# Optimization experiments

Hardware: AMD Instinct MI355X
Metric: run time of the kernel (lower is better)

Reference implementation:

```python
import jax, jax.numpy as jnp
import numpy as np

B, T_MAX, D_MODEL, H, DH = 16, 4096, 1024, 16, 64


def _rope(x, positions):
    """Standard half-split RoPE. x: (B, T, H, Dh), positions: (T,) int32."""
    half = x.shape[-1] // 2
    inv_freq = 1.0 / (10000.0 ** (jnp.arange(half, dtype=jnp.float32) / half))
    ang = positions.astype(jnp.float32)[:, None] * inv_freq  # (T, half)
    cos = jnp.cos(ang)[None, :, None, :]  # (1, T, 1, half)
    sin = jnp.sin(ang)[None, :, None, :]
    x1, x2 = x[..., :half], x[..., half:]
    return jnp.concatenate([x1 * cos - x2 * sin, x1 * sin + x2 * cos], axis=-1)


def setup_inputs() -> dict:
    key = jax.random.key(0)
    ks = jax.random.split(key, 8)
    s_in = 1.0 / np.sqrt(D_MODEL)
    s_out = 1.0 / np.sqrt(H * DH)
    return {
        "x": jax.random.normal(ks[0], (B, 1, D_MODEL), jnp.float32),
        "cached_key": jax.random.normal(ks[1], (B, T_MAX, H, DH), jnp.float32),
        "cached_value": jax.random.normal(ks[2], (B, T_MAX, H, DH), jnp.float32),
        "Wq": jax.random.normal(ks[3], (D_MODEL, H, DH), jnp.float32) * s_in,
        "bq": jnp.zeros((H, DH), jnp.float32),
        "Wk": jax.random.normal(ks[4], (D_MODEL, H, DH), jnp.float32) * s_in,
        "bk": jnp.zeros((H, DH), jnp.float32),
        "Wv": jax.random.normal(ks[5], (D_MODEL, H, DH), jnp.float32) * s_in,
        "bv": jnp.zeros((H, DH), jnp.float32),
        "Wo": jax.random.normal(ks[6], (H, DH, D_MODEL), jnp.float32) * s_out,
        "bo": jnp.zeros((D_MODEL,), jnp.float32),
        "cache_index": 2047,
    }


def reference(x, cached_key, cached_value, Wq, bq, Wk, bk, Wv, bv, Wo, bo, cache_index):
    # QKV projections on the single decode token: (B, 1, H, Dh)
    q = jnp.einsum('bte,ehd->bthd', x, Wq) + bq
    k = jnp.einsum('bte,ehd->bthd', x, Wk) + bk
    v = jnp.einsum('bte,ehd->bthd', x, Wv) + bv

    # Scatter new K/V into the fixed cache at cache_index
    ck = cached_key.at[:, cache_index].set(k[:, 0])
    cv = cached_value.at[:, cache_index].set(v[:, 0])

    # RoPE: Q at position cache_index, K over the entire cache 0..T_max-1
    q_rot = _rope(q, jnp.array([cache_index], dtype=jnp.int32))
    k_rot = _rope(ck, jnp.arange(T_MAX, dtype=jnp.int32))

    # Masked single-query dot-product attention over valid slots
    scale = 1.0 / np.sqrt(DH).astype(np.float32)
    scores = jnp.einsum('bqhd,bkhd->bhqk', q_rot, k_rot) * scale  # (B, H, 1, T)
    slot_mask = jnp.arange(T_MAX) <= cache_index  # (T,)
    scores = jnp.where(slot_mask[None, None, None, :], scores, jnp.float32(-1e30))
    attn = jax.nn.softmax(scores, axis=-1)
    o = jnp.einsum('bhqk,bkhd->bqhd', attn, cv)  # (B, 1, H, Dh)

    # Output projection
    return jnp.einsum('bqhd,hde->bqe', o, Wo) + bo  # (B, 1, d_model)
```

## Files before the change

kernel.cpp:

```cpp
#include <hip/hip_runtime.h>
#include <math.h>

typedef float f4 __attribute__((ext_vector_type(4)));

#define B_    16
#define TMAX  4096
#define DM    1024
#define H_    16
#define DH    64
#define SPLIT 8
#define SCALE 0.125f
#define ROPE_L 0.28782313662425572f

#define WS_Q     0
#define WS_PO    16384
#define WS_PM    147456
#define WS_PL    149504
#define WS_OF    151552
#define WS_BIG   167936

__device__ __forceinline__ f4 ldnt(const f4* p) { return __builtin_nontemporal_load(p); }

__device__ __forceinline__ float wred_max(float v) {
#pragma unroll
    for (int o = 32; o > 0; o >>= 1) v = fmaxf(v, __shfl_xor(v, o, 64));
    return v;
}
__device__ __forceinline__ float wred_sum(float v) {
#pragma unroll
    for (int o = 32; o > 0; o >>= 1) v += __shfl_xor(v, o, 64);
    return v;
}

__global__ __launch_bounds__(256) void k_qkv(const float* __restrict__ x,
                      const float* __restrict__ Wq, const float* __restrict__ Wk,
                      const float* __restrict__ Wv, float* __restrict__ ws) {
    const int ec = blockIdx.x, h = blockIdx.y, mat = blockIdx.z;
    const float* W = (mat == 0) ? Wq : ((mat == 1) ? Wk : Wv);
    const int tid = threadIdx.x;
    const int d = tid & 63, es = tid >> 6;
    __shared__ float xs[B_][128];
    __shared__ float red[4][B_][64];
    for (int i = tid; i < B_ * 128; i += 256) {
        int b = i >> 7, e = i & 127;
        xs[b][e] = x[b * DM + ec * 128 + e];
    }
    __syncthreads();
    float acc[B_];
#pragma unroll
    for (int b = 0; b < B_; b++) acc[b] = 0.f;
    for (int i = 0; i < 32; i++) {
        int el = es * 32 + i;
        int e = ec * 128 + el;
        float w = W[((size_t)e * H_ + h) * DH + d];
#pragma unroll
        for (int b = 0; b < B_; b++) acc[b] += xs[b][el] * w;
    }
#pragma unroll
    for (int b = 0; b < B_; b++) red[es][b][d] = acc[b];
    __syncthreads();
    const int b4 = tid >> 6;
#pragma unroll
    for (int bb = 0; bb < 4; bb++) {
        int b = b4 * 4 + bb;
        float v = red[0][b][d] + red[1][b][d] + red[2][b][d] + red[3][b][d];
        ws[WS_BIG + (((size_t)(mat * 8 + ec) * B_ + b) * H_ + h) * DH + d] = v;
    }
}

__global__ void k_qkvred(float* __restrict__ cached_key, float* __restrict__ cached_value,
                         const float* __restrict__ bq, const float* __restrict__ bk,
                         const float* __restrict__ bv, const int* __restrict__ cidx,
                         float* __restrict__ ws) {
    const int bh = blockIdx.x, d = threadIdx.x;
    const int b = bh >> 4, h = bh & 15;
    const int P = *cidx;
    float q = bq[h * 64 + d], k = bk[h * 64 + d], v = bv[h * 64 + d];
    const float* big = ws + WS_BIG;
    const size_t matstride = (size_t)8 * B_ * H_ * DH;
#pragma unroll
    for (int ec = 0; ec < 8; ec++) {
        size_t base = (((size_t)ec * B_ + b) * H_ + h) * DH + d;
        q += big[base];
        k += big[matstride + base];
        v += big[2 * matstride + base];
    }
    ws[WS_Q + bh * 64 + d] = q;
    size_t off = (((size_t)b * TMAX + P) * H_ + h) * DH + d;
    cached_key[off] = k;
    cached_value[off] = v;
}

__global__ __launch_bounds__(256) void k_attn(const float* __restrict__ K,
                                              const float* __restrict__ V,
                                              const int* __restrict__ cidx,
                                              float* __restrict__ ws) {
    const int s = blockIdx.x, h = blockIdx.y, b = blockIdx.z;
    const int tid = threadIdx.x;
    const int P = *cidx;
    const int n = P + 1;
    const int chunk = (n + SPLIT - 1) / SPLIT;
    const int t0 = s * chunk;
    int t1 = t0 + chunk; if (t1 > n) t1 = n;
    const int len = (t1 > t0) ? (t1 - t0) : 0;
    const int bh = b * H_ + h;

    __shared__ float qr[64];
    __shared__ float sc[512];
    __shared__ float rb_m[4], rb_s[4];
    __shared__ float ov[16][64];

    if (tid < 64) {
        int d = tid;
        const float* qv = ws + WS_Q + bh * 64;
        int j = (d < 32) ? d : (d - 32);
        float invf = __expf(-(float)j * ROPE_L);
        float sn, c;
        sincosf((float)P * invf, &sn, &c);
        qr[d] = (d < 32) ? (qv[d] * c - qv[d + 32] * sn)
                         : (qv[d - 32] * sn + qv[d] * c);
    }
    __syncthreads();

    const int pos_sub = tid >> 3, q = tid & 7;
    float qa0 = qr[4 * q + 0], qa1 = qr[4 * q + 1], qa2 = qr[4 * q + 2], qa3 = qr[4 * q + 3];
    float qb0 = qr[4 * q + 32], qb1 = qr[4 * q + 33], qb2 = qr[4 * q + 34], qb3 = qr[4 * q + 35];
    float if0 = __expf(-(float)(4 * q + 0) * ROPE_L);
    float if1 = __expf(-(float)(4 * q + 1) * ROPE_L);
    float if2 = __expf(-(float)(4 * q + 2) * ROPE_L);
    float if3 = __expf(-(float)(4 * q + 3) * ROPE_L);

    float tmax = -3.0e38f;
    for (int base = 0; base < len; base += 32) {
        int idx = base + pos_sub;
        bool act = idx < len;
        int t = t0 + idx;
        f4 k1 = {0.f, 0.f, 0.f, 0.f}, k2 = {0.f, 0.f, 0.f, 0.f};
        if (act) {
            const f4* kp = (const f4*)(K + (((size_t)b * TMAX + t) * H_ + h) * DH);
            k1 = ldnt(kp + q);
            k2 = ldnt(kp + q + 8);
        }
        float tf = (float)t;
        float s0, c0, s1, c1, s2, c2, s3, c3;
        sincosf(tf * if0, &s0, &c0);
        sincosf(tf * if1, &s1, &c1);
        sincosf(tf * if2, &s2, &c2);
        sincosf(tf * if3, &s3, &c3);
        float p = k1.x * (qa0 * c0 + qb0 * s0) + k2.x * (qb0 * c0 - qa0 * s0)
                + k1.y * (qa1 * c1 + qb1 * s1) + k2.y * (qb1 * c1 - qa1 * s1)
                + k1.z * (qa2 * c2 + qb2 * s2) + k2.z * (qb2 * c2 - qa2 * s2)
                + k1.w * (qa3 * c3 + qb3 * s3) + k2.w * (qb3 * c3 - qa3 * s3);
#pragma unroll
        for (int o = 1; o < 8; o <<= 1) p += __shfl_xor(p, o, 64);
        if (act) {
            float sv = p * SCALE;
            if (q == 0) sc[idx] = sv;
            tmax = fmaxf(tmax, sv);
        }
    }
    float wm = wred_max(tmax);
    if ((tid & 63) == 0) rb_m[tid >> 6] = wm;
    __syncthreads();
    float m = fmaxf(fmaxf(rb_m[0], rb_m[1]), fmaxf(rb_m[2], rb_m[3]));

    float tsum = 0.f;
    for (int idx = tid; idx < len; idx += 256) {
        float pp = __expf(sc[idx] - m);
        sc[idx] = pp;
        tsum += pp;
    }
    float wsum = wred_sum(tsum);
    if ((tid & 63) == 0) rb_s[tid >> 6] = wsum;
    __syncthreads();
    float l = rb_s[0] + rb_s[1] + rb_s[2] + rb_s[3];

    const int d4 = tid & 15, grp = tid >> 4;
    f4 acc4 = {0.f, 0.f, 0.f, 0.f};
#pragma unroll 4
    for (int idx = grp; idx < len; idx += 16) {
        int t = t0 + idx;
        const f4* vp = (const f4*)(V + (((size_t)b * TMAX + t) * H_ + h) * DH) + d4;
        f4 vv = ldnt(vp);
        acc4 += sc[idx] * vv;
    }
    *(f4*)&ov[grp][d4 * 4] = acc4;
    __syncthreads();
    if (tid < 64) {
        float o = 0.f;
#pragma unroll
        for (int g = 0; g < 16; g++) o += ov[g][tid];
        ws[WS_PO + ((size_t)bh * SPLIT + s) * 64 + tid] = o;
        if (tid == 0) {
            ws[WS_PM + bh * SPLIT + s] = (len > 0) ? m : -1.0e30f;
            ws[WS_PL + bh * SPLIT + s] = l;
        }
    }
}

__global__ void k_combine(float* __restrict__ ws) {
    int bh = blockIdx.x;
    int d = threadIdx.x;
    const float* pm = ws + WS_PM + bh * SPLIT;
    const float* pl = ws + WS_PL + bh * SPLIT;
    const float* po = ws + WS_PO + (size_t)bh * SPLIT * 64;
    float m = -3.0e38f;
#pragma unroll
    for (int s = 0; s < SPLIT; s++) m = fmaxf(m, pm[s]);
    float l = 0.f, o = 0.f;
#pragma unroll
    for (int s = 0; s < SPLIT; s++) {
        float w = __expf(pm[s] - m);
        l += pl[s] * w;
        o += po[s * 64 + d] * w;
    }
    ws[WS_OF + bh * 64 + d] = o / l;
}

__global__ __launch_bounds__(256) void k_oproj(const float* __restrict__ Wo,
                        float* __restrict__ ws) {
    const int ec = blockIdx.x, hc = blockIdx.y;
    const int tid = threadIdx.x;
    const int el = tid & 63, grp = tid >> 6;
    const int e = ec * 64 + el;
    __shared__ float ofs[B_][64];
    __shared__ float red[4][B_][64];
    for (int i = tid; i < B_ * 64; i += 256) {
        int b = i >> 6, j = i & 63;
        ofs[b][j] = ws[WS_OF + b * (H_ * DH) + hc * 64 + j];
    }
    __syncthreads();
    float acc[B_];
#pragma unroll
    for (int b = 0; b < B_; b++) acc[b] = 0.f;
    for (int i = 0; i < 16; i++) {
        int hl = grp * 16 + i;
        int hd = hc * 64 + hl;
        float w = Wo[(size_t)hd * DM + e];
#pragma unroll
        for (int b = 0; b < B_; b++) acc[b] += ofs[b][hl] * w;
    }
#pragma unroll
    for (int b = 0; b < B_; b++) red[grp][b][el] = acc[b];
    __syncthreads();
    const int b4 = tid >> 6;
#pragma unroll
    for (int bb = 0; bb < 4; bb++) {
        int b = b4 * 4 + bb;
        float v = red[0][b][el] + red[1][b][el] + red[2][b][el] + red[3][b][el];
        ws[WS_BIG + ((size_t)hc * B_ + b) * DM + ec * 64 + el] = v;
    }
}

__global__ void k_out(const float* __restrict__ bo, const float* __restrict__ ws,
                      float* __restrict__ out) {
    int idx = blockIdx.x * 256 + threadIdx.x;
    int e = idx & (DM - 1);
    float v = bo[e];
#pragma unroll
    for (int hc = 0; hc < 16; hc++) v += ws[WS_BIG + (size_t)hc * B_ * DM + idx];
    out[idx] = v;
}

extern "C" void kernel_launch(void* const* d_in, const int* in_sizes, int n_in,
                              void* d_out, int out_size, void* d_ws, size_t ws_size,
                              hipStream_t stream) {
    const float* x  = (const float*)d_in[0];
    float* ck       = (float*)d_in[1];
    float* cv       = (float*)d_in[2];
    const float* Wq = (const float*)d_in[3];
    const float* bq = (const float*)d_in[4];
    const float* Wk = (const float*)d_in[5];
    const float* bk = (const float*)d_in[6];
    const float* Wv = (const float*)d_in[7];
    const float* bv = (const float*)d_in[8];
    const float* Wo = (const float*)d_in[9];
    const float* bo = (const float*)d_in[10];
    const int* cidx = (const int*)d_in[11];
    float* ws  = (float*)d_ws;
    float* out = (float*)d_out;

    k_qkv<<<dim3(8, H_, 3), 256, 0, stream>>>(x, Wq, Wk, Wv, ws);
    k_qkvred<<<B_ * H_, 64, 0, stream>>>(ck, cv, bq, bk, bv, cidx, ws);
    k_attn<<<dim3(SPLIT, H_, B_), 256, 0, stream>>>(ck, cv, cidx, ws);
    k_combine<<<B_ * H_, 64, 0, stream>>>(ws);
    k_oproj<<<dim3(16, 16), 256, 0, stream>>>(Wo, ws);
    k_out<<<64, 256, 0, stream>>>(bo, ws, out);
}
```

Measured before the change: 480.1 us.

## Fuse QKV reduction into attention and output sum into output projection

Removes the separate QKV-reduce kernel by having attention blocks reduce Q (and K/V for the block owning the new position) directly. The new K/V row is served from shared memory instead of being written to the cache. The final cross-chunk sum kernel is removed by having each oproj block loop over all head chunks and write output with bias. This saves launches and workspace traffic but cuts the oproj grid from 256 to 16 blocks, lowering parallelism on the Wo read.

```diff
diff --git a/kernel.cpp b/kernel.cpp
--- a/kernel.cpp
+++ b/kernel.cpp
@@ -12,7 +12,6 @@
 #define SCALE 0.125f
 #define ROPE_L 0.28782313662425572f
 
-#define WS_Q     0
 #define WS_PO    16384
 #define WS_PM    147456
 #define WS_PL    149504
@@ -68,31 +67,11 @@
     }
 }
 
-__global__ void k_qkvred(float* __restrict__ cached_key, float* __restrict__ cached_value,
-                         const float* __restrict__ bq, const float* __restrict__ bk,
-                         const float* __restrict__ bv, const int* __restrict__ cidx,
-                         float* __restrict__ ws) {
-    const int bh = blockIdx.x, d = threadIdx.x;
-    const int b = bh >> 4, h = bh & 15;
-    const int P = *cidx;
-    float q = bq[h * 64 + d], k = bk[h * 64 + d], v = bv[h * 64 + d];
-    const float* big = ws + WS_BIG;
-    const size_t matstride = (size_t)8 * B_ * H_ * DH;
-#pragma unroll
-    for (int ec = 0; ec < 8; ec++) {
-        size_t base = (((size_t)ec * B_ + b) * H_ + h) * DH + d;
-        q += big[base];
-        k += big[matstride + base];
-        v += big[2 * matstride + base];
-    }
-    ws[WS_Q + bh * 64 + d] = q;
-    size_t off = (((size_t)b * TMAX + P) * H_ + h) * DH + d;
-    cached_key[off] = k;
-    cached_value[off] = v;
-}
-
 __global__ __launch_bounds__(256) void k_attn(const float* __restrict__ K,
                                               const float* __restrict__ V,
+                                              const float* __restrict__ bq,
+                                              const float* __restrict__ bk,
+                                              const float* __restrict__ bv,
                                               const int* __restrict__ cidx,
                                               float* __restrict__ ws) {
     const int s = blockIdx.x, h = blockIdx.y, b = blockIdx.z;
@@ -104,21 +83,40 @@
     int t1 = t0 + chunk; if (t1 > n) t1 = n;
     const int len = (t1 > t0) ? (t1 - t0) : 0;
     const int bh = b * H_ + h;
+    const bool hasP = (P >= t0) && (P < t1);
 
     __shared__ float qr[64];
+    __shared__ float kPs[64];
+    __shared__ float vPs[64];
     __shared__ float sc[512];
     __shared__ float rb_m[4], rb_s[4];
     __shared__ float ov[16][64];
 
     if (tid < 64) {
-        int d = tid;
-        const float* qv = ws + WS_Q + bh * 64;
+        const int d = tid;
+        const float* big = ws + WS_BIG;
+        const size_t matstride = (size_t)8 * B_ * H_ * DH;
+        float q = bq[h * 64 + d];
+#pragma unroll
+        for (int ec = 0; ec < 8; ec++)
+            q += big[(((size_t)ec * B_ + b) * H_ + h) * DH + d];
         int j = (d < 32) ? d : (d - 32);
         float invf = __expf(-(float)j * ROPE_L);
         float sn, c;
         sincosf((float)P * invf, &sn, &c);
-        qr[d] = (d < 32) ? (qv[d] * c - qv[d + 32] * sn)
-                         : (qv[d - 32] * sn + qv[d] * c);
+        float qp = __shfl_xor(q, 32, 64);
+        qr[d] = (d < 32) ? (q * c - qp * sn) : (qp * sn + q * c);
+        if (hasP) {
+            float kk = bk[h * 64 + d], vv = bv[h * 64 + d];
+#pragma unroll
+            for (int ec = 0; ec < 8; ec++) {
+                size_t base = (((size_t)ec * B_ + b) * H_ + h) * DH + d;
+                kk += big[matstride + base];
+                vv += big[2 * matstride + base];
+            }
+            kPs[d] = kk;
+            vPs[d] = vv;
+        }
     }
     __syncthreads();
 
@@ -137,9 +135,15 @@
         int t = t0 + idx;
         f4 k1 = {0.f, 0.f, 0.f, 0.f}, k2 = {0.f, 0.f, 0.f, 0.f};
         if (act) {
-            const f4* kp = (const f4*)(K + (((size_t)b * TMAX + t) * H_ + h) * DH);
-            k1 = ldnt(kp + q);
-            k2 = ldnt(kp + q + 8);
+            if (t == P) {
+                const f4* kp = (const f4*)kPs;
+                k1 = kp[q];
+                k2 = kp[q + 8];
+            } else {
+                const f4* kp = (const f4*)(K + (((size_t)b * TMAX + t) * H_ + h) * DH);
+                k1 = ldnt(kp + q);
+                k2 = ldnt(kp + q + 8);
+            }
         }
         float tf = (float)t;
         float s0, c0, s1, c1, s2, c2, s3, c3;
@@ -180,8 +184,12 @@
 #pragma unroll 4
     for (int idx = grp; idx < len; idx += 16) {
         int t = t0 + idx;
-        const f4* vp = (const f4*)(V + (((size_t)b * TMAX + t) * H_ + h) * DH) + d4;
-        f4 vv = ldnt(vp);
+        f4 vv;
+        if (t == P) {
+            vv = ((const f4*)vPs)[d4];
+        } else {
+            vv = ldnt((const f4*)(V + (((size_t)b * TMAX + t) * H_ + h) * DH) + d4);
+        }
         acc4 += sc[idx] * vv;
     }
     *(f4*)&ov[grp][d4 * 4] = acc4;
@@ -218,56 +226,51 @@
 }
 
 __global__ __launch_bounds__(256) void k_oproj(const float* __restrict__ Wo,
-                        float* __restrict__ ws) {
-    const int ec = blockIdx.x, hc = blockIdx.y;
+                                               const float* __restrict__ bo,
+                                               const float* __restrict__ ws,
+                                               float* __restrict__ out) {
+    const int ec = blockIdx.x;
     const int tid = threadIdx.x;
     const int el = tid & 63, grp = tid >> 6;
     const int e = ec * 64 + el;
     __shared__ float ofs[B_][64];
     __shared__ float red[4][B_][64];
-    for (int i = tid; i < B_ * 64; i += 256) {
-        int b = i >> 6, j = i & 63;
-        ofs[b][j] = ws[WS_OF + b * (H_ * DH) + hc * 64 + j];
-    }
-    __syncthreads();
     float acc[B_];
 #pragma unroll
     for (int b = 0; b < B_; b++) acc[b] = 0.f;
-    for (int i = 0; i < 16; i++) {
-        int hl = grp * 16 + i;
-        int hd = hc * 64 + hl;
-        float w = Wo[(size_t)hd * DM + e];
-#pragma unroll
-        for (int b = 0; b < B_; b++) acc[b] += ofs[b][hl] * w;
+    for (int hc = 0; hc < 16; hc++) {
+        for (int i = tid; i < B_ * 64; i += 256) {
+            int b = i >> 6, j = i & 63;
+            ofs[b][j] = ws[WS_OF + b * (H_ * DH) + hc * 64 + j];
+        }
+        __syncthreads();
+        for (int i = 0; i < 16; i++) {
+            int hl = grp * 16 + i;
+            float w = Wo[(size_t)(hc * 64 + hl) * DM + e];
+#pragma unroll
+            for (int b = 0; b < B_; b++) acc[b] += ofs[b][hl] * w;
+        }
+        __syncthreads();
     }
 #pragma unroll
     for (int b = 0; b < B_; b++) red[grp][b][el] = acc[b];
     __syncthreads();
     const int b4 = tid >> 6;
+    float bias = bo[e];
 #pragma unroll
     for (int bb = 0; bb < 4; bb++) {
         int b = b4 * 4 + bb;
         float v = red[0][b][el] + red[1][b][el] + red[2][b][el] + red[3][b][el];
-        ws[WS_BIG + ((size_t)hc * B_ + b) * DM + ec * 64 + el] = v;
-    }
-}
-
-__global__ void k_out(const float* __restrict__ bo, const float* __restrict__ ws,
-                      float* __restrict__ out) {
-    int idx = blockIdx.x * 256 + threadIdx.x;
-    int e = idx & (DM - 1);
-    float v = bo[e];
-#pragma unroll
-    for (int hc = 0; hc < 16; hc++) v += ws[WS_BIG + (size_t)hc * B_ * DM + idx];
-    out[idx] = v;
+        out[(size_t)b * DM + e] = bias + v;
+    }
 }
 
 extern "C" void kernel_launch(void* const* d_in, const int* in_sizes, int n_in,
                               void* d_out, int out_size, void* d_ws, size_t ws_size,
                               hipStream_t stream) {
     const float* x  = (const float*)d_in[0];
-    float* ck       = (float*)d_in[1];
-    float* cv       = (float*)d_in[2];
+    const float* ck = (const float*)d_in[1];
+    const float* cv = (const float*)d_in[2];
     const float* Wq = (const float*)d_in[3];
     const float* bq = (const float*)d_in[4];
     const float* Wk = (const float*)d_in[5];
@@ -281,9 +284,7 @@
     float* out = (float*)d_out;
 
     k_qkv<<<dim3(8, H_, 3), 256, 0, stream>>>(x, Wq, Wk, Wv, ws);
-    k_qkvred<<<B_ * H_, 64, 0, stream>>>(ck, cv, bq, bk, bv, cidx, ws);
-    k_attn<<<dim3(SPLIT, H_, B_), 256, 0, stream>>>(ck, cv, cidx, ws);
+    k_attn<<<dim3(SPLIT, H_, B_), 256, 0, stream>>>(ck, cv, bq, bk, bv, cidx, ws);
     k_combine<<<B_ * H_, 64, 0, stream>>>(ws);
-    k_oproj<<<dim3(16, 16), 256, 0, stream>>>(Wo, ws);
-    k_out<<<64, 256, 0, stream>>>(bo, ws, out);
-}
+    k_oproj<<<dim3(16), 256, 0, stream>>>(Wo, bo, ws, out);
+}
```

Measured after the change: 525.6 us. +9.5%, slower.
